# Kernel tuning notes

Hardware: AMD Instinct MI355X
Metric: run time of the kernel (lower is better)

Reference implementation:

```python
import jax, jax.numpy as jnp
import numpy as np

M, N = 4096, 4096  # placement density grid size (even, as the rfft-based kernel assumes)


def _expk(L):
    # precompute_expk(L): [cos(pi*k/(2L)), sin(pi*k/(2L))] stacked -> [L, 2]
    a = np.pi * np.arange(L) / (2.0 * L)
    return np.stack([np.cos(a), np.sin(a)], axis=-1).astype(np.float32)


def setup_inputs() -> dict:
    key = jax.random.key(0)
    x = jax.random.normal(key, (M, N), dtype=jnp.float32)
    return {
        "x": x,
        "expkM": jnp.asarray(_expk(M)),
        "expkN": jnp.asarray(_expk(N)),
    }


def _idct1d(x, expk):
    # Unnormalized IDCT (DCT-III with DC weight 1) along the last axis:
    #   y_u = sum_k x_k * cos(pi*k*(2u+1)/(2L))
    # Makhoul FFT trick: c_k = x_k * exp(i*pi*k/(2L)); v = L*ifft(c);
    #   y[2m] = Re(v[m]),  y[2m+1] = Re(v[L-1-m])
    L = x.shape[-1]
    ek = expk[:, 0] + 1j * expk[:, 1]            # exp(i*pi*k/(2L)), [L]
    v = (jnp.fft.ifft(x * ek, axis=-1) * L).real  # [..., L]
    half = L // 2
    even = v[..., :half]                          # y[0], y[2], ...
    odd = v[..., ::-1][..., :half]                # y[1], y[3], ... (= v[L-1], v[L-2], ...)
    return jnp.stack([even, odd], axis=-1).reshape(x.shape)


def reference(x, expkM, expkN):
    # out[u,v] = sum_{p,q} x[p,q] cos(pi*p*(2u+1)/(2M)) cos(pi*q*(2v+1)/(2N))
    t = _idct1d(x, expkN)                               # transform along N (last dim)
    out = _idct1d(t.swapaxes(-1, -2), expkM)            # transform along M
    return out.swapaxes(-1, -2)
```

## Files before the change

kernel.cpp:

```cpp
#include <hip/hip_runtime.h>
#include <stdint.h>

typedef __bf16 bf16x8_t __attribute__((ext_vector_type(8)));
typedef float f32x4_t __attribute__((ext_vector_type(4)));

__device__ __forceinline__ uint32_t f32_to_bf16_bits(float f) {
    union { float f; uint32_t u; } v; v.f = f;
    return (v.u + 0x7FFFu + ((v.u >> 16) & 1u)) >> 16;
}

__global__ void prep_kernel(const float* __restrict__ X,
                            unsigned short* __restrict__ Ae,
                            unsigned short* __restrict__ Ao,
                            unsigned short* __restrict__ Xe,
                            unsigned short* __restrict__ Xo) {
    if (blockIdx.x < 4096) {
        const int idx = blockIdx.x * 256 + threadIdx.x;
        const int sel = idx >> 19;
        const int e   = idx & ((1 << 19) - 1);
        const int n   = e >> 8;
        const int c0  = (e & 255) << 3;
        const uint32_t tn = (uint32_t)(2 * n + 1);
        unsigned short* dst = sel ? Ao : Ae;
        uint32_t packed[4];
#pragma unroll
        for (int jj = 0; jj < 4; ++jj) {
            uint32_t cA = (uint32_t)(c0 + 2 * jj);
            uint32_t cB = cA + 1;
            uint32_t r0 = ((2u * cA + (uint32_t)sel) * tn) & 16383u;
            uint32_t r1 = ((2u * cB + (uint32_t)sel) * tn) & 16383u;
            float v0 = __cosf((float)r0 * 3.8349519697141e-4f);
            float v1 = __cosf((float)r1 * 3.8349519697141e-4f);
            packed[jj] = f32_to_bf16_bits(v0) | (f32_to_bf16_bits(v1) << 16);
        }
        *(uint4*)(dst + (size_t)n * 2048 + c0) = make_uint4(packed[0], packed[1], packed[2], packed[3]);
    } else {
        const int idx = (blockIdx.x - 4096) * 256 + threadIdx.x;
        const int q   = idx >> 9;
        const int p0  = (idx & 511) << 3;
        const float4* src = (const float4*)(X + (size_t)q * 4096 + p0);
        float4 a = src[0];
        float4 b = src[1];
        uint2 ev, od;
        ev.x = f32_to_bf16_bits(a.x) | (f32_to_bf16_bits(a.z) << 16);
        ev.y = f32_to_bf16_bits(b.x) | (f32_to_bf16_bits(b.z) << 16);
        od.x = f32_to_bf16_bits(a.y) | (f32_to_bf16_bits(a.w) << 16);
        od.y = f32_to_bf16_bits(b.y) | (f32_to_bf16_bits(b.w) << 16);
        *(uint2*)(Xe + (size_t)q * 2048 + (p0 >> 1)) = ev;
        *(uint2*)(Xo + (size_t)q * 2048 + (p0 >> 1)) = od;
    }
}

#define GLL(gp, lp) __builtin_amdgcn_global_load_lds( \
        (const __attribute__((address_space(1))) uint32_t*)(gp), \
        (__attribute__((address_space(3))) uint32_t*)(lp), 16, 0, 0)

#define STAGE8(buf, gA, gB, kadv) do {                                        \
    _Pragma("unroll")                                                         \
    for (int k_ = 0; k_ < 4; ++k_) {                                          \
        GLL((gA) + (kadv) + src_off[k_], (buf) + uldsb[k_]);                  \
        GLL((gB) + (kadv) + src_off[k_], (buf) + 8192 + uldsb[k_]);           \
    }                                                                         \
} while (0)

#define COMPUTE_TILE(buf, acc) do {                                           \
    const unsigned short* lA_ = (buf);                                        \
    const unsigned short* lB_ = (buf) + 8192;                                 \
    _Pragma("unroll")                                                         \
    for (int kh_ = 0; kh_ < 2; ++kh_) {                                       \
        const int so_ = (((kh_ << 2) + gq) ^ sw) << 3;                        \
        bf16x8_t af_[4], bf_[4];                                              \
        _Pragma("unroll")                                                     \
        for (int i_ = 0; i_ < 4; ++i_) af_[i_] = *(const bf16x8_t*)(lA_ + aRow + i_ * 1024 + so_); \
        _Pragma("unroll")                                                     \
        for (int j_ = 0; j_ < 4; ++j_) bf_[j_] = *(const bf16x8_t*)(lB_ + bRow + j_ * 1024 + so_); \
        __builtin_amdgcn_s_setprio(1);                                        \
        _Pragma("unroll")                                                     \
        for (int i_ = 0; i_ < 4; ++i_)                                        \
            _Pragma("unroll")                                                 \
            for (int j_ = 0; j_ < 4; ++j_)                                    \
                acc[i_][j_] = __builtin_amdgcn_mfma_f32_16x16x32_bf16(af_[i_], bf_[j_], acc[i_][j_], 0, 0, 0); \
        __builtin_amdgcn_s_setprio(0);                                        \
    }                                                                         \
} while (0)

#define TILE_SYNC() do {                                                      \
    asm volatile("s_waitcnt vmcnt(0)" ::: "memory");                          \
    __builtin_amdgcn_s_barrier();                                             \
    asm volatile("" ::: "memory");                                            \
} while (0)

template <int STAGE>
__global__ __launch_bounds__(256, 2)
void gemm_fused_kernel(const unsigned short* __restrict__ Ae,
                       const unsigned short* __restrict__ Ao,
                       const unsigned short* __restrict__ Re,
                       const unsigned short* __restrict__ Ro,
                       unsigned short* __restrict__ Te,
                       unsigned short* __restrict__ To,
                       float* __restrict__ out) {
    constexpr int KD = 2048;
    __shared__ __attribute__((aligned(16))) unsigned short smem[2 * 16384];

    const int tid  = threadIdx.x;
    const int wave = tid >> 6;
    const int lane = tid & 63;

    const int tile_m = blockIdx.y << 7;
    const int tile_c = blockIdx.x << 7;

    const unsigned short* pAe = Ae + (size_t)tile_m * KD;
    const unsigned short* pAo = Ao + (size_t)tile_m * KD;
    const unsigned short* pBe = Re + (size_t)tile_c * KD;
    const unsigned short* pBo = Ro + (size_t)tile_c * KD;

    f32x4_t acc_e[4][4], acc_o[4][4];
#pragma unroll
    for (int i = 0; i < 4; ++i)
#pragma unroll
        for (int j = 0; j < 4; ++j) {
            acc_e[i][j] = (f32x4_t){0.f, 0.f, 0.f, 0.f};
            acc_o[i][j] = (f32x4_t){0.f, 0.f, 0.f, 0.f};
        }

    int src_off[4], uldsb[4];
#pragma unroll
    for (int k = 0; k < 4; ++k) {
        const int c   = (wave << 6) + lane + (k << 8);
        const int row = c >> 3;
        const int g   = (c & 7) ^ (row & 7);
        src_off[k] = row * KD + (g << 3);
        uldsb[k]   = ((wave << 6) + (k << 8)) << 3;
    }

    const int frow = lane & 15;
    const int sw   = frow & 7;
    const int gq   = lane >> 4;
    const int aRow = ((wave >> 1) * 64 + frow) * 64;
    const int bRow = ((wave & 1) * 64 + frow) * 64;

    STAGE8(smem, pAe, pBe, 0);
    TILE_SYNC();

    int co = 0;
#pragma unroll 1
    for (int t = 0; t < 31; ++t) {
        STAGE8(smem + (co ^ 16384), pAe, pBe, (size_t)(t + 1) << 6);
        COMPUTE_TILE(smem + co, acc_e);
        TILE_SYNC();
        co ^= 16384;
    }
    STAGE8(smem + (co ^ 16384), pAo, pBo, 0);
    COMPUTE_TILE(smem + co, acc_e);
    TILE_SYNC();
    co ^= 16384;
#pragma unroll 1
    for (int t = 0; t < 31; ++t) {
        STAGE8(smem + (co ^ 16384), pAo, pBo, (size_t)(t + 1) << 6);
        COMPUTE_TILE(smem + co, acc_o);
        TILE_SYNC();
        co ^= 16384;
    }
    COMPUTE_TILE(smem + co, acc_o);

    const int orow = tile_m + (wave >> 1) * 64 + ((lane >> 4) << 2);
    const int ocol = tile_c + (wave & 1) * 64 + (lane & 15);
    if (STAGE == 1) {
        unsigned short* dst = (ocol & 1) ? To : Te;
#pragma unroll
        for (int i = 0; i < 4; ++i)
#pragma unroll
            for (int j = 0; j < 4; ++j)
#pragma unroll
                for (int r = 0; r < 4; ++r) {
                    const int n = orow + i * 16 + r;
                    const int c = (ocol + j * 16) >> 1;
                    const float e = acc_e[i][j][r], o = acc_o[i][j][r];
                    dst[(size_t)n * 2048 + c]          = (unsigned short)f32_to_bf16_bits(e + o);
                    dst[(size_t)(4095 - n) * 2048 + c] = (unsigned short)f32_to_bf16_bits(e - o);
                }
    } else {
#pragma unroll
        for (int i = 0; i < 4; ++i)
#pragma unroll
            for (int j = 0; j < 4; ++j)
#pragma unroll
                for (int r = 0; r < 4; ++r) {
                    const int m = orow + i * 16 + r;
                    const int w = ocol + j * 16;
                    const float e = acc_e[i][j][r], o = acc_o[i][j][r];
                    out[(size_t)m * 4096 + w]          = e + o;
                    out[(size_t)(4095 - m) * 4096 + w] = e - o;
                }
    }
}

extern "C" void kernel_launch(void* const* d_in, const int* in_sizes, int n_in,
                              void* d_out, int out_size, void* d_ws, size_t ws_size,
                              hipStream_t stream) {
    const float* x = (const float*)d_in[0];
    char* ws = (char*)d_ws;
    const size_t MB = 1024 * 1024;
    unsigned short* Ae = (unsigned short*)(ws);
    unsigned short* Ao = (unsigned short*)(ws + 8 * MB);
    unsigned short* Xe = (unsigned short*)(ws + 16 * MB);
    unsigned short* Xo = (unsigned short*)(ws + 32 * MB);
    unsigned short* Te = (unsigned short*)(ws + 48 * MB);
    unsigned short* To = (unsigned short*)(ws + 64 * MB);
    float* out = (float*)d_out;

    prep_kernel<<<12288, 256, 0, stream>>>(x, Ae, Ao, Xe, Xo);

    dim3 grid(32, 16);
    gemm_fused_kernel<1><<<grid, 256, 0, stream>>>(Ae, Ao, Xe, Xo, Te, To, nullptr);
    gemm_fused_kernel<2><<<grid, 256, 0, stream>>>(Ae, Ao, Te, To, nullptr, nullptr, out);
}
```

Baseline: 252.6 us.

## Split fused even/odd GEMM into 256x256-tile GEMMs plus separate butterfly kernels

Replaces the 128x128 fused GEMM, which accumulated the even and odd halves in one block and did the butterfly in its epilogue, with a 256x256-tile, 512-thread GEMM. The even/odd parity now runs as separate grid z-slices, and the GEMM writes bf16 intermediate products. Separate bfly1/bfly2 kernels then combine the even and odd results with vectorized loads and stores. The larger tiles are meant to raise arithmetic intensity and give the GEMM vectorizable stores, at the cost of extra launches, an extra bf16 round trip through memory, and one more bf16 rounding of the intermediates.

After: 261.9 us. +3.7%, slower.

```diff
diff --git a/kernel.cpp b/kernel.cpp
--- a/kernel.cpp
+++ b/kernel.cpp
@@ -7,6 +7,11 @@
 __device__ __forceinline__ uint32_t f32_to_bf16_bits(float f) {
     union { float f; uint32_t u; } v; v.f = f;
     return (v.u + 0x7FFFu + ((v.u >> 16) & 1u)) >> 16;
+}
+
+__device__ __forceinline__ float bf16_bits_to_f32(uint32_t b) {
+    union { uint32_t u; float f; } v; v.u = b << 16;
+    return v.f;
 }
 
 __global__ void prep_kernel(const float* __restrict__ X,
@@ -55,28 +60,74 @@
         (const __attribute__((address_space(1))) uint32_t*)(gp), \
         (__attribute__((address_space(3))) uint32_t*)(lp), 16, 0, 0)
 
-#define STAGE8(buf, gA, gB, kadv) do {                                        \
+__global__ __launch_bounds__(512, 2)
+void gemm256_kernel(const unsigned short* __restrict__ Ae,
+                    const unsigned short* __restrict__ Ao,
+                    const unsigned short* __restrict__ Be,
+                    const unsigned short* __restrict__ Bo,
+                    unsigned short* __restrict__ Ce,
+                    unsigned short* __restrict__ Co) {
+    constexpr int KD = 2048;
+    __shared__ __attribute__((aligned(16))) unsigned short smem[2 * 32768];
+
+    const int tid  = threadIdx.x;
+    const int wave = tid >> 6;
+    const int lane = tid & 63;
+    const int wm   = wave >> 2;
+    const int wn   = wave & 3;
+
+    const int tile_m = blockIdx.y << 8;
+    const int tile_c = blockIdx.x << 8;
+    const int par    = blockIdx.z;
+
+    const unsigned short* gA = (par ? Ao : Ae) + (size_t)tile_m * KD;
+    const unsigned short* gB = (par ? Bo : Be) + (size_t)tile_c * KD;
+    unsigned short*       gC = par ? Co : Ce;
+
+    f32x4_t acc[8][4];
+#pragma unroll
+    for (int i = 0; i < 8; ++i)
+#pragma unroll
+        for (int j = 0; j < 4; ++j)
+            acc[i][j] = (f32x4_t){0.f, 0.f, 0.f, 0.f};
+
+    int src_off[4], lds_off[4];
+#pragma unroll
+    for (int k = 0; k < 4; ++k) {
+        const int c   = tid + (k << 9);
+        const int row = c >> 3;
+        const int g   = (c & 7) ^ (row & 7);
+        src_off[k] = row * KD + (g << 3);
+        lds_off[k] = c << 3;
+    }
+
+    const int frow = lane & 15;
+    const int sw   = frow & 7;
+    const int gq   = lane >> 4;
+    const int aRowB = (wm * 128 + frow) * 64;
+    const int bRowB = (wn * 64  + frow) * 64;
+
+#define STAGE_TILE(buf, kadv) do {                                            \
     _Pragma("unroll")                                                         \
-    for (int k_ = 0; k_ < 4; ++k_) {                                          \
-        GLL((gA) + (kadv) + src_off[k_], (buf) + uldsb[k_]);                  \
-        GLL((gB) + (kadv) + src_off[k_], (buf) + 8192 + uldsb[k_]);           \
-    }                                                                         \
+    for (int k_ = 0; k_ < 4; ++k_)                                            \
+        GLL(gA + (kadv) + src_off[k_], (buf) + lds_off[k_]);                  \
+    _Pragma("unroll")                                                         \
+    for (int k_ = 0; k_ < 4; ++k_)                                            \
+        GLL(gB + (kadv) + src_off[k_], (buf) + 16384 + lds_off[k_]);          \
 } while (0)
 
-#define COMPUTE_TILE(buf, acc) do {                                           \
-    const unsigned short* lA_ = (buf);                                        \
-    const unsigned short* lB_ = (buf) + 8192;                                 \
+#define COMPUTE_TILE(buf) do {                                                \
     _Pragma("unroll")                                                         \
     for (int kh_ = 0; kh_ < 2; ++kh_) {                                       \
         const int so_ = (((kh_ << 2) + gq) ^ sw) << 3;                        \
-        bf16x8_t af_[4], bf_[4];                                              \
+        bf16x8_t af_[8], bf_[4];                                              \
         _Pragma("unroll")                                                     \
-        for (int i_ = 0; i_ < 4; ++i_) af_[i_] = *(const bf16x8_t*)(lA_ + aRow + i_ * 1024 + so_); \
+        for (int i_ = 0; i_ < 8; ++i_) af_[i_] = *(const bf16x8_t*)((buf) + aRowB + i_ * 1024 + so_); \
         _Pragma("unroll")                                                     \
-        for (int j_ = 0; j_ < 4; ++j_) bf_[j_] = *(const bf16x8_t*)(lB_ + bRow + j_ * 1024 + so_); \
+        for (int j_ = 0; j_ < 4; ++j_) bf_[j_] = *(const bf16x8_t*)((buf) + 16384 + bRowB + j_ * 1024 + so_); \
         __builtin_amdgcn_s_setprio(1);                                        \
         _Pragma("unroll")                                                     \
-        for (int i_ = 0; i_ < 4; ++i_)                                        \
+        for (int i_ = 0; i_ < 8; ++i_)                                        \
             _Pragma("unroll")                                                 \
             for (int j_ = 0; j_ < 4; ++j_)                                    \
                 acc[i_][j_] = __builtin_amdgcn_mfma_f32_16x16x32_bf16(af_[i_], bf_[j_], acc[i_][j_], 0, 0, 0); \
@@ -90,108 +141,94 @@
     asm volatile("" ::: "memory");                                            \
 } while (0)
 
-template <int STAGE>
-__global__ __launch_bounds__(256, 2)
-void gemm_fused_kernel(const unsigned short* __restrict__ Ae,
-                       const unsigned short* __restrict__ Ao,
-                       const unsigned short* __restrict__ Re,
-                       const unsigned short* __restrict__ Ro,
-                       unsigned short* __restrict__ Te,
-                       unsigned short* __restrict__ To,
-                       float* __restrict__ out) {
-    constexpr int KD = 2048;
-    __shared__ __attribute__((aligned(16))) unsigned short smem[2 * 16384];
-
-    const int tid  = threadIdx.x;
-    const int wave = tid >> 6;
-    const int lane = tid & 63;
-
-    const int tile_m = blockIdx.y << 7;
-    const int tile_c = blockIdx.x << 7;
-
-    const unsigned short* pAe = Ae + (size_t)tile_m * KD;
-    const unsigned short* pAo = Ao + (size_t)tile_m * KD;
-    const unsigned short* pBe = Re + (size_t)tile_c * KD;
-    const unsigned short* pBo = Ro + (size_t)tile_c * KD;
-
-    f32x4_t acc_e[4][4], acc_o[4][4];
-#pragma unroll
-    for (int i = 0; i < 4; ++i)
-#pragma unroll
-        for (int j = 0; j < 4; ++j) {
-            acc_e[i][j] = (f32x4_t){0.f, 0.f, 0.f, 0.f};
-            acc_o[i][j] = (f32x4_t){0.f, 0.f, 0.f, 0.f};
-        }
-
-    int src_off[4], uldsb[4];
-#pragma unroll
-    for (int k = 0; k < 4; ++k) {
-        const int c   = (wave << 6) + lane + (k << 8);
-        const int row = c >> 3;
-        const int g   = (c & 7) ^ (row & 7);
-        src_off[k] = row * KD + (g << 3);
-        uldsb[k]   = ((wave << 6) + (k << 8)) << 3;
-    }
-
-    const int frow = lane & 15;
-    const int sw   = frow & 7;
-    const int gq   = lane >> 4;
-    const int aRow = ((wave >> 1) * 64 + frow) * 64;
-    const int bRow = ((wave & 1) * 64 + frow) * 64;
-
-    STAGE8(smem, pAe, pBe, 0);
+    STAGE_TILE(smem, 0);
     TILE_SYNC();
 
     int co = 0;
 #pragma unroll 1
     for (int t = 0; t < 31; ++t) {
-        STAGE8(smem + (co ^ 16384), pAe, pBe, (size_t)(t + 1) << 6);
-        COMPUTE_TILE(smem + co, acc_e);
+        STAGE_TILE(smem + (co ^ 32768), (size_t)(t + 1) << 6);
+        COMPUTE_TILE(smem + co);
         TILE_SYNC();
-        co ^= 16384;
-    }
-    STAGE8(smem + (co ^ 16384), pAo, pBo, 0);
-    COMPUTE_TILE(smem + co, acc_e);
-    TILE_SYNC();
-    co ^= 16384;
-#pragma unroll 1
-    for (int t = 0; t < 31; ++t) {
-        STAGE8(smem + (co ^ 16384), pAo, pBo, (size_t)(t + 1) << 6);
-        COMPUTE_TILE(smem + co, acc_o);
-        TILE_SYNC();
-        co ^= 16384;
-    }
-    COMPUTE_TILE(smem + co, acc_o);
-
-    const int orow = tile_m + (wave >> 1) * 64 + ((lane >> 4) << 2);
-    const int ocol = tile_c + (wave & 1) * 64 + (lane & 15);
-    if (STAGE == 1) {
-        unsigned short* dst = (ocol & 1) ? To : Te;
-#pragma unroll
-        for (int i = 0; i < 4; ++i)
-#pragma unroll
-            for (int j = 0; j < 4; ++j)
-#pragma unroll
-                for (int r = 0; r < 4; ++r) {
-                    const int n = orow + i * 16 + r;
-                    const int c = (ocol + j * 16) >> 1;
-                    const float e = acc_e[i][j][r], o = acc_o[i][j][r];
-                    dst[(size_t)n * 2048 + c]          = (unsigned short)f32_to_bf16_bits(e + o);
-                    dst[(size_t)(4095 - n) * 2048 + c] = (unsigned short)f32_to_bf16_bits(e - o);
-                }
-    } else {
-#pragma unroll
-        for (int i = 0; i < 4; ++i)
-#pragma unroll
-            for (int j = 0; j < 4; ++j)
-#pragma unroll
-                for (int r = 0; r < 4; ++r) {
-                    const int m = orow + i * 16 + r;
-                    const int w = ocol + j * 16;
-                    const float e = acc_e[i][j][r], o = acc_o[i][j][r];
-                    out[(size_t)m * 4096 + w]          = e + o;
-                    out[(size_t)(4095 - m) * 4096 + w] = e - o;
-                }
+        co ^= 32768;
+    }
+    COMPUTE_TILE(smem + co);
+
+#undef STAGE_TILE
+#undef COMPUTE_TILE
+#undef TILE_SYNC
+
+    const int orow = tile_m + wm * 128 + ((lane >> 4) << 2);
+    const int ocol = tile_c + wn * 64 + (lane & 15);
+#pragma unroll
+    for (int i = 0; i < 8; ++i)
+#pragma unroll
+        for (int j = 0; j < 4; ++j)
+#pragma unroll
+            for (int r = 0; r < 4; ++r) {
+                const int m = orow + i * 16 + r;
+                const int w = ocol + j * 16;
+                gC[(size_t)m * 4096 + w] = (unsigned short)f32_to_bf16_bits(acc[i][j][r]);
+            }
+}
+
+__global__ void bfly1_kernel(const unsigned short* __restrict__ Ce,
+                             const unsigned short* __restrict__ Co,
+                             unsigned short* __restrict__ Te,
+                             unsigned short* __restrict__ To) {
+    const int m  = blockIdx.x;
+    const int c0 = threadIdx.x << 4;
+    const uint4 e0 = *(const uint4*)(Ce + (size_t)m * 4096 + c0);
+    const uint4 e1 = *(const uint4*)(Ce + (size_t)m * 4096 + c0 + 8);
+    const uint4 o0 = *(const uint4*)(Co + (size_t)m * 4096 + c0);
+    const uint4 o1 = *(const uint4*)(Co + (size_t)m * 4096 + c0 + 8);
+    const uint32_t eu[8] = {e0.x, e0.y, e0.z, e0.w, e1.x, e1.y, e1.z, e1.w};
+    const uint32_t ou[8] = {o0.x, o0.y, o0.z, o0.w, o1.x, o1.y, o1.z, o1.w};
+    uint32_t se[4], so_[4], de[4], do_[4];
+#pragma unroll
+    for (int u = 0; u < 4; ++u) {
+        float eA = bf16_bits_to_f32(eu[2*u] & 0xFFFF),  oA = bf16_bits_to_f32(ou[2*u] & 0xFFFF);
+        float eB = bf16_bits_to_f32(eu[2*u] >> 16),     oB = bf16_bits_to_f32(ou[2*u] >> 16);
+        float eC = bf16_bits_to_f32(eu[2*u+1] & 0xFFFF),oC = bf16_bits_to_f32(ou[2*u+1] & 0xFFFF);
+        float eD = bf16_bits_to_f32(eu[2*u+1] >> 16),   oD = bf16_bits_to_f32(ou[2*u+1] >> 16);
+        se[u]  = f32_to_bf16_bits(eA + oA) | (f32_to_bf16_bits(eC + oC) << 16);
+        so_[u] = f32_to_bf16_bits(eB + oB) | (f32_to_bf16_bits(eD + oD) << 16);
+        de[u]  = f32_to_bf16_bits(eA - oA) | (f32_to_bf16_bits(eC - oC) << 16);
+        do_[u] = f32_to_bf16_bits(eB - oB) | (f32_to_bf16_bits(eD - oD) << 16);
+    }
+    const size_t rs = (size_t)m * 2048 + (c0 >> 1);
+    const size_t rd = (size_t)(4095 - m) * 2048 + (c0 >> 1);
+    *(uint4*)(Te + rs) = make_uint4(se[0], se[1], se[2], se[3]);
+    *(uint4*)(To + rs) = make_uint4(so_[0], so_[1], so_[2], so_[3]);
+    *(uint4*)(Te + rd) = make_uint4(de[0], de[1], de[2], de[3]);
+    *(uint4*)(To + rd) = make_uint4(do_[0], do_[1], do_[2], do_[3]);
+}
+
+__global__ void bfly2_kernel(const unsigned short* __restrict__ Ce,
+                             const unsigned short* __restrict__ Co,
+                             float* __restrict__ out) {
+    const int m  = blockIdx.x;
+    const int c0 = threadIdx.x << 4;
+    const uint4 e0 = *(const uint4*)(Ce + (size_t)m * 4096 + c0);
+    const uint4 e1 = *(const uint4*)(Ce + (size_t)m * 4096 + c0 + 8);
+    const uint4 o0 = *(const uint4*)(Co + (size_t)m * 4096 + c0);
+    const uint4 o1 = *(const uint4*)(Co + (size_t)m * 4096 + c0 + 8);
+    const uint32_t eu[8] = {e0.x, e0.y, e0.z, e0.w, e1.x, e1.y, e1.z, e1.w};
+    const uint32_t ou[8] = {o0.x, o0.y, o0.z, o0.w, o1.x, o1.y, o1.z, o1.w};
+    float s[16], d[16];
+#pragma unroll
+    for (int u = 0; u < 8; ++u) {
+        const float eL = bf16_bits_to_f32(eu[u] & 0xFFFF), oL = bf16_bits_to_f32(ou[u] & 0xFFFF);
+        const float eH = bf16_bits_to_f32(eu[u] >> 16),    oH = bf16_bits_to_f32(ou[u] >> 16);
+        s[2*u] = eL + oL; s[2*u+1] = eH + oH;
+        d[2*u] = eL - oL; d[2*u+1] = eH - oH;
+    }
+    float* ps = out + (size_t)m * 4096 + c0;
+    float* pd = out + (size_t)(4095 - m) * 4096 + c0;
+#pragma unroll
+    for (int u = 0; u < 4; ++u) {
+        *(float4*)(ps + 4 * u) = make_float4(s[4*u], s[4*u+1], s[4*u+2], s[4*u+3]);
+        *(float4*)(pd + 4 * u) = make_float4(d[4*u], d[4*u+1], d[4*u+2], d[4*u+3]);
     }
 }
 
@@ -205,13 +242,15 @@
     unsigned short* Ao = (unsigned short*)(ws + 8 * MB);
     unsigned short* Xe = (unsigned short*)(ws + 16 * MB);
     unsigned short* Xo = (unsigned short*)(ws + 32 * MB);
-    unsigned short* Te = (unsigned short*)(ws + 48 * MB);
-    unsigned short* To = (unsigned short*)(ws + 64 * MB);
+    unsigned short* C1e = (unsigned short*)(ws + 48 * MB);
+    unsigned short* C1o = (unsigned short*)(ws + 64 * MB);
     float* out = (float*)d_out;
 
     prep_kernel<<<12288, 256, 0, stream>>>(x, Ae, Ao, Xe, Xo);
 
-    dim3 grid(32, 16);
-    gemm_fused_kernel<1><<<grid, 256, 0, stream>>>(Ae, Ao, Xe, Xo, Te, To, nullptr);
-    gemm_fused_kernel<2><<<grid, 256, 0, stream>>>(Ae, Ao, Te, To, nullptr, nullptr, out);
-}
+    dim3 ggrid(16, 8, 2);
+    gemm256_kernel<<<ggrid, 512, 0, stream>>>(Ae, Ao, Xe, Xo, C1e, C1o);
+    bfly1_kernel<<<2048, 256, 0, stream>>>(C1e, C1o, Xe, Xo);
+    gemm256_kernel<<<ggrid, 512, 0, stream>>>(Ae, Ao, Xe, Xo, C1e, C1o);
+    bfly2_kernel<<<2048, 256, 0, stream>>>(C1e, C1o, out);
+}
```

## Enlarge GEMM block tile to 128x256 with eight waves per block

Applied to the files above, without the earlier changes.

Each GEMM block now covers a 128x256 output tile using 512 threads (2x4 waves), where it previously covered 128x128 with 256 threads. The A tile staged in LDS is now shared by twice as many B columns, which cuts global/L2 traffic for A per output. The grid is halved to 256 blocks, and LDS per block grows to 96 KB for double buffering, which limits occupancy and leaves fewer blocks to spread across CUs.

Result: slower. 259.3 us (+2.7%).

```diff
diff --git a/kernel.cpp b/kernel.cpp
--- a/kernel.cpp
+++ b/kernel.cpp
@@ -55,25 +55,83 @@
         (const __attribute__((address_space(1))) uint32_t*)(gp), \
         (__attribute__((address_space(3))) uint32_t*)(lp), 16, 0, 0)
 
-#define STAGE8(buf, gA, gB, kadv) do {                                        \
-    _Pragma("unroll")                                                         \
-    for (int k_ = 0; k_ < 4; ++k_) {                                          \
-        GLL((gA) + (kadv) + src_off[k_], (buf) + uldsb[k_]);                  \
-        GLL((gB) + (kadv) + src_off[k_], (buf) + 8192 + uldsb[k_]);           \
-    }                                                                         \
+template <int STAGE>
+__global__ __launch_bounds__(512, 2)
+void gemm_fused_kernel(const unsigned short* __restrict__ Ae,
+                       const unsigned short* __restrict__ Ao,
+                       const unsigned short* __restrict__ Re,
+                       const unsigned short* __restrict__ Ro,
+                       unsigned short* __restrict__ Te,
+                       unsigned short* __restrict__ To,
+                       float* __restrict__ out) {
+    constexpr int KD = 2048;
+    __shared__ __attribute__((aligned(16))) unsigned short smem[2 * 24576];
+
+    const int tid  = threadIdx.x;
+    const int wave = tid >> 6;
+    const int lane = tid & 63;
+    const int wm   = wave >> 2;
+    const int wn   = wave & 3;
+
+    const int tile_m = blockIdx.y << 7;
+    const int tile_c = blockIdx.x << 8;
+
+    const unsigned short* pAe = Ae + (size_t)tile_m * KD;
+    const unsigned short* pAo = Ao + (size_t)tile_m * KD;
+    const unsigned short* pBe = Re + (size_t)tile_c * KD;
+    const unsigned short* pBo = Ro + (size_t)tile_c * KD;
+
+    f32x4_t acc_e[4][4], acc_o[4][4];
+#pragma unroll
+    for (int i = 0; i < 4; ++i)
+#pragma unroll
+        for (int j = 0; j < 4; ++j) {
+            acc_e[i][j] = (f32x4_t){0.f, 0.f, 0.f, 0.f};
+            acc_o[i][j] = (f32x4_t){0.f, 0.f, 0.f, 0.f};
+        }
+
+    int a_src[2], a_lds[2], b_src[4], b_lds[4];
+#pragma unroll
+    for (int k = 0; k < 2; ++k) {
+        const int c   = tid + (k << 9);
+        const int row = c >> 3;
+        const int g   = (c & 7) ^ (row & 7);
+        a_src[k] = row * KD + (g << 3);
+        a_lds[k] = c << 3;
+    }
+#pragma unroll
+    for (int k = 0; k < 4; ++k) {
+        const int c   = tid + (k << 9);
+        const int row = c >> 3;
+        const int g   = (c & 7) ^ (row & 7);
+        b_src[k] = row * KD + (g << 3);
+        b_lds[k] = 8192 + (c << 3);
+    }
+
+    const int frow = lane & 15;
+    const int sw   = frow & 7;
+    const int gq   = lane >> 4;
+    const int aRow = (wm * 64 + frow) * 64;
+    const int bRow = 8192 + (wn * 64 + frow) * 64;
+
+#define STAGE_TILE(buf, gA, gB, kadv) do {                                    \
+    GLL((gA) + (kadv) + a_src[0], (buf) + a_lds[0]);                          \
+    GLL((gA) + (kadv) + a_src[1], (buf) + a_lds[1]);                          \
+    GLL((gB) + (kadv) + b_src[0], (buf) + b_lds[0]);                          \
+    GLL((gB) + (kadv) + b_src[1], (buf) + b_lds[1]);                          \
+    GLL((gB) + (kadv) + b_src[2], (buf) + b_lds[2]);                          \
+    GLL((gB) + (kadv) + b_src[3], (buf) + b_lds[3]);                          \
 } while (0)
 
 #define COMPUTE_TILE(buf, acc) do {                                           \
-    const unsigned short* lA_ = (buf);                                        \
-    const unsigned short* lB_ = (buf) + 8192;                                 \
     _Pragma("unroll")                                                         \
     for (int kh_ = 0; kh_ < 2; ++kh_) {                                       \
         const int so_ = (((kh_ << 2) + gq) ^ sw) << 3;                        \
         bf16x8_t af_[4], bf_[4];                                              \
         _Pragma("unroll")                                                     \
-        for (int i_ = 0; i_ < 4; ++i_) af_[i_] = *(const bf16x8_t*)(lA_ + aRow + i_ * 1024 + so_); \
+        for (int i_ = 0; i_ < 4; ++i_) af_[i_] = *(const bf16x8_t*)((buf) + aRow + i_ * 1024 + so_); \
         _Pragma("unroll")                                                     \
-        for (int j_ = 0; j_ < 4; ++j_) bf_[j_] = *(const bf16x8_t*)(lB_ + bRow + j_ * 1024 + so_); \
+        for (int j_ = 0; j_ < 4; ++j_) bf_[j_] = *(const bf16x8_t*)((buf) + bRow + j_ * 1024 + so_); \
         __builtin_amdgcn_s_setprio(1);                                        \
         _Pragma("unroll")                                                     \
         for (int i_ = 0; i_ < 4; ++i_)                                        \
@@ -90,81 +148,36 @@
     asm volatile("" ::: "memory");                                            \
 } while (0)
 
-template <int STAGE>
-__global__ __launch_bounds__(256, 2)
-void gemm_fused_kernel(const unsigned short* __restrict__ Ae,
-                       const unsigned short* __restrict__ Ao,
-                       const unsigned short* __restrict__ Re,
-                       const unsigned short* __restrict__ Ro,
-                       unsigned short* __restrict__ Te,
-                       unsigned short* __restrict__ To,
-                       float* __restrict__ out) {
-    constexpr int KD = 2048;
-    __shared__ __attribute__((aligned(16))) unsigned short smem[2 * 16384];
-
-    const int tid  = threadIdx.x;
-    const int wave = tid >> 6;
-    const int lane = tid & 63;
-
-    const int tile_m = blockIdx.y << 7;
-    const int tile_c = blockIdx.x << 7;
-
-    const unsigned short* pAe = Ae + (size_t)tile_m * KD;
-    const unsigned short* pAo = Ao + (size_t)tile_m * KD;
-    const unsigned short* pBe = Re + (size_t)tile_c * KD;
-    const unsigned short* pBo = Ro + (size_t)tile_c * KD;
-
-    f32x4_t acc_e[4][4], acc_o[4][4];
-#pragma unroll
-    for (int i = 0; i < 4; ++i)
-#pragma unroll
-        for (int j = 0; j < 4; ++j) {
-            acc_e[i][j] = (f32x4_t){0.f, 0.f, 0.f, 0.f};
-            acc_o[i][j] = (f32x4_t){0.f, 0.f, 0.f, 0.f};
-        }
-
-    int src_off[4], uldsb[4];
-#pragma unroll
-    for (int k = 0; k < 4; ++k) {
-        const int c   = (wave << 6) + lane + (k << 8);
-        const int row = c >> 3;
-        const int g   = (c & 7) ^ (row & 7);
-        src_off[k] = row * KD + (g << 3);
-        uldsb[k]   = ((wave << 6) + (k << 8)) << 3;
-    }
-
-    const int frow = lane & 15;
-    const int sw   = frow & 7;
-    const int gq   = lane >> 4;
-    const int aRow = ((wave >> 1) * 64 + frow) * 64;
-    const int bRow = ((wave & 1) * 64 + frow) * 64;
-
-    STAGE8(smem, pAe, pBe, 0);
+    STAGE_TILE(smem, pAe, pBe, 0);
     TILE_SYNC();
 
     int co = 0;
 #pragma unroll 1
     for (int t = 0; t < 31; ++t) {
-        STAGE8(smem + (co ^ 16384), pAe, pBe, (size_t)(t + 1) << 6);
+        STAGE_TILE(smem + (co ^ 24576), pAe, pBe, (t + 1) << 6);
         COMPUTE_TILE(smem + co, acc_e);
         TILE_SYNC();
-        co ^= 16384;
-    }
-    STAGE8(smem + (co ^ 16384), pAo, pBo, 0);
+        co ^= 24576;
+    }
+    STAGE_TILE(smem + (co ^ 24576), pAo, pBo, 0);
     COMPUTE_TILE(smem + co, acc_e);
     TILE_SYNC();
-    co ^= 16384;
+    co ^= 24576;
 #pragma unroll 1
     for (int t = 0; t < 31; ++t) {
-        STAGE8(smem + (co ^ 16384), pAo, pBo, (size_t)(t + 1) << 6);
+        STAGE_TILE(smem + (co ^ 24576), pAo, pBo, (t + 1) << 6);
         COMPUTE_TILE(smem + co, acc_o);
         TILE_SYNC();
-        co ^= 16384;
+        co ^= 24576;
     }
     COMPUTE_TILE(smem + co, acc_o);
 
-    const int orow = tile_m + (wave >> 1) * 64 + ((lane >> 4) << 2);
-    const int ocol = tile_c + (wave & 1) * 64 + (lane & 15);
+#undef STAGE_TILE
+#undef COMPUTE_TILE
+#undef TILE_SYNC
+
+    const int orow = tile_m + wm * 64 + ((lane >> 4) << 2);
+    const int ocol = tile_c + wn * 64 + (lane & 15);
     if (STAGE == 1) {
         unsigned short* dst = (ocol & 1) ? To : Te;
 #pragma unroll
@@ -211,7 +224,7 @@
 
     prep_kernel<<<12288, 256, 0, stream>>>(x, Ae, Ao, Xe, Xo);
 
-    dim3 grid(32, 16);
-    gemm_fused_kernel<1><<<grid, 256, 0, stream>>>(Ae, Ao, Xe, Xo, Te, To, nullptr);
-    gemm_fused_kernel<2><<<grid, 256, 0, stream>>>(Ae, Ao, Te, To, nullptr, nullptr, out);
-}
+    dim3 grid(16, 16);
+    gemm_fused_kernel<1><<<grid, 512, 0, stream>>>(Ae, Ao, Xe, Xo, Te, To, nullptr);
+    gemm_fused_kernel<2><<<grid, 512, 0, stream>>>(Ae, Ao, Te, To, nullptr, nullptr, out);
+}
```

## Pre-swizzle cosine matrix into MFMA fragment order and load A directly from global

Applied to the files above, without the earlier changes.

The prep kernel now writes the cosine basis matrices in an MFMA-fragment-major layout, so each lane's 8-element A fragment is contiguous. The GEMM then reads A fragments straight from global memory (through the cache) instead of staging them through LDS, which halves LDS traffic and LDS footprint per block. The trade-off is that A loads are now synchronous global loads issued inside the compute loop, no longer prefetched a tile ahead, so their latency may be exposed.

New measurement: 279.1 us. +10.5%, slower.

```diff
diff --git a/kernel.cpp b/kernel.cpp
--- a/kernel.cpp
+++ b/kernel.cpp
@@ -18,22 +18,27 @@
         const int idx = blockIdx.x * 256 + threadIdx.x;
         const int sel = idx >> 19;
         const int e   = idx & ((1 << 19) - 1);
-        const int n   = e >> 8;
-        const int c0  = (e & 255) << 3;
+        const int ln  = e & 63;
+        const int kh  = (e >> 6) & 1;
+        const int ii  = (e >> 7) & 3;
+        const int kt  = (e >> 9) & 31;
+        const int blk = (e >> 14) & 31;
+        const int n   = blk * 64 + ii * 16 + (ln & 15);
+        const int r0  = kt * 64 + kh * 32 + (ln >> 4) * 8;
         const uint32_t tn = (uint32_t)(2 * n + 1);
         unsigned short* dst = sel ? Ao : Ae;
         uint32_t packed[4];
 #pragma unroll
         for (int jj = 0; jj < 4; ++jj) {
-            uint32_t cA = (uint32_t)(c0 + 2 * jj);
+            uint32_t cA = (uint32_t)(r0 + 2 * jj);
             uint32_t cB = cA + 1;
-            uint32_t r0 = ((2u * cA + (uint32_t)sel) * tn) & 16383u;
-            uint32_t r1 = ((2u * cB + (uint32_t)sel) * tn) & 16383u;
-            float v0 = __cosf((float)r0 * 3.8349519697141e-4f);
-            float v1 = __cosf((float)r1 * 3.8349519697141e-4f);
+            uint32_t q0 = ((2u * cA + (uint32_t)sel) * tn) & 16383u;
+            uint32_t q1 = ((2u * cB + (uint32_t)sel) * tn) & 16383u;
+            float v0 = __cosf((float)q0 * 3.8349519697141e-4f);
+            float v1 = __cosf((float)q1 * 3.8349519697141e-4f);
             packed[jj] = f32_to_bf16_bits(v0) | (f32_to_bf16_bits(v1) << 16);
         }
-        *(uint4*)(dst + (size_t)n * 2048 + c0) = make_uint4(packed[0], packed[1], packed[2], packed[3]);
+        *(uint4*)(dst + (size_t)e * 8) = make_uint4(packed[0], packed[1], packed[2], packed[3]);
     } else {
         const int idx = (blockIdx.x - 4096) * 256 + threadIdx.x;
         const int q   = idx >> 9;
@@ -55,25 +60,23 @@
         (const __attribute__((address_space(1))) uint32_t*)(gp), \
         (__attribute__((address_space(3))) uint32_t*)(lp), 16, 0, 0)
 
-#define STAGE8(buf, gA, gB, kadv) do {                                        \
+#define STAGE4(buf, gB, kadv) do {                                            \
     _Pragma("unroll")                                                         \
-    for (int k_ = 0; k_ < 4; ++k_) {                                          \
-        GLL((gA) + (kadv) + src_off[k_], (buf) + uldsb[k_]);                  \
-        GLL((gB) + (kadv) + src_off[k_], (buf) + 8192 + uldsb[k_]);           \
-    }                                                                         \
+    for (int k_ = 0; k_ < 4; ++k_)                                            \
+        GLL((gB) + (kadv) + src_off[k_], (buf) + uldsb[k_]);                  \
 } while (0)
 
-#define COMPUTE_TILE(buf, acc) do {                                           \
-    const unsigned short* lA_ = (buf);                                        \
-    const unsigned short* lB_ = (buf) + 8192;                                 \
+#define COMPUTE_TILE(buf, acc, pA, ktv) do {                                  \
+    const unsigned short* aT_ = (pA) + aMB + (size_t)(ktv) * 4096;            \
     _Pragma("unroll")                                                         \
     for (int kh_ = 0; kh_ < 2; ++kh_) {                                       \
-        const int so_ = (((kh_ << 2) + gq) ^ sw) << 3;                        \
         bf16x8_t af_[4], bf_[4];                                              \
         _Pragma("unroll")                                                     \
-        for (int i_ = 0; i_ < 4; ++i_) af_[i_] = *(const bf16x8_t*)(lA_ + aRow + i_ * 1024 + so_); \
+        for (int i_ = 0; i_ < 4; ++i_)                                        \
+            af_[i_] = *(const bf16x8_t*)(aT_ + (i_ * 2 + kh_) * 512 + aLane); \
+        const int so_ = (((kh_ << 2) + gq) ^ sw) << 3;                        \
         _Pragma("unroll")                                                     \
-        for (int j_ = 0; j_ < 4; ++j_) bf_[j_] = *(const bf16x8_t*)(lB_ + bRow + j_ * 1024 + so_); \
+        for (int j_ = 0; j_ < 4; ++j_) bf_[j_] = *(const bf16x8_t*)((buf) + bRow + j_ * 1024 + so_); \
         __builtin_amdgcn_s_setprio(1);                                        \
         _Pragma("unroll")                                                     \
         for (int i_ = 0; i_ < 4; ++i_)                                        \
@@ -100,7 +103,7 @@
                        unsigned short* __restrict__ To,
                        float* __restrict__ out) {
     constexpr int KD = 2048;
-    __shared__ __attribute__((aligned(16))) unsigned short smem[2 * 16384];
+    __shared__ __attribute__((aligned(16))) unsigned short smem[2 * 8192];
 
     const int tid  = threadIdx.x;
     const int wave = tid >> 6;
@@ -109,10 +112,11 @@
     const int tile_m = blockIdx.y << 7;
     const int tile_c = blockIdx.x << 7;
 
-    const unsigned short* pAe = Ae + (size_t)tile_m * KD;
-    const unsigned short* pAo = Ao + (size_t)tile_m * KD;
     const unsigned short* pBe = Re + (size_t)tile_c * KD;
     const unsigned short* pBo = Ro + (size_t)tile_c * KD;
+
+    const size_t aMB  = (size_t)((blockIdx.y << 1) + (wave >> 1)) * (32 * 4096);
+    const int    aLane = lane << 3;
 
     f32x4_t acc_e[4][4], acc_o[4][4];
 #pragma unroll
@@ -136,32 +140,31 @@
     const int frow = lane & 15;
     const int sw   = frow & 7;
     const int gq   = lane >> 4;
-    const int aRow = ((wave >> 1) * 64 + frow) * 64;
     const int bRow = ((wave & 1) * 64 + frow) * 64;
 
-    STAGE8(smem, pAe, pBe, 0);
+    STAGE4(smem, pBe, 0);
     TILE_SYNC();
 
     int co = 0;
 #pragma unroll 1
     for (int t = 0; t < 31; ++t) {
-        STAGE8(smem + (co ^ 16384), pAe, pBe, (size_t)(t + 1) << 6);
-        COMPUTE_TILE(smem + co, acc_e);
+        STAGE4(smem + (co ^ 8192), pBe, (size_t)(t + 1) << 6);
+        COMPUTE_TILE(smem + co, acc_e, Ae, t);
         TILE_SYNC();
-        co ^= 16384;
-    }
-    STAGE8(smem + (co ^ 16384), pAo, pBo, 0);
-    COMPUTE_TILE(smem + co, acc_e);
+        co ^= 8192;
+    }
+    STAGE4(smem + (co ^ 8192), pBo, 0);
+    COMPUTE_TILE(smem + co, acc_e, Ae, 31);
     TILE_SYNC();
-    co ^= 16384;
+    co ^= 8192;
 #pragma unroll 1
     for (int t = 0; t < 31; ++t) {
-        STAGE8(smem + (co ^ 16384), pAo, pBo, (size_t)(t + 1) << 6);
-        COMPUTE_TILE(smem + co, acc_o);
+        STAGE4(smem + (co ^ 8192), pBo, (size_t)(t + 1) << 6);
+        COMPUTE_TILE(smem + co, acc_o, Ao, t);
         TILE_SYNC();
-        co ^= 16384;
-    }
-    COMPUTE_TILE(smem + co, acc_o);
+        co ^= 8192;
+    }
+    COMPUTE_TILE(smem + co, acc_o, Ao, 31);
 
     const int orow = tile_m + (wave >> 1) * 64 + ((lane >> 4) << 2);
     const int ocol = tile_c + (wave & 1) * 64 + (lane & 15);
```
